# Optimization experiments

Hardware: AMD Instinct MI355X
Metric: run time of the kernel (lower is better)

## Reference

```python
import jax, jax.numpy as jnp
import numpy as np

EMB_DIM = 1024
N_HEADS = 16
HEAD_DIM = EMB_DIM // N_HEADS


def setup_inputs() -> dict:
    key = jax.random.key(0)
    ks = jax.random.split(key, 6)
    B, S, D = 2, 2048, EMB_DIM
    s = 1.0 / np.sqrt(D)
    return {
        "x": jax.random.normal(ks[0], (B, S, D), dtype=jnp.float32),
        "wq": jax.random.normal(ks[1], (D, D), dtype=jnp.float32) * s,
        "wk": jax.random.normal(ks[2], (D, D), dtype=jnp.float32) * s,
        "wv": jax.random.normal(ks[3], (D, D), dtype=jnp.float32) * s,
        "wo": jax.random.normal(ks[4], (D, D), dtype=jnp.float32) * s,
        "bo": jax.random.normal(ks[5], (D,), dtype=jnp.float32) * 0.01,
    }


def reference(x, wq, wk, wv, wo, bo):
    B, S, D = x.shape
    H, Hd = N_HEADS, HEAD_DIM
    # projections (torch Linear: y = x @ W.T; here weights are stored as [in, out])
    q = (x @ wq).reshape(B, S, H, Hd).transpose(0, 2, 1, 3)  # [B,H,S,Hd]
    k = (x @ wk).reshape(B, S, H, Hd).transpose(0, 2, 1, 3)
    v = (x @ wv).reshape(B, S, H, Hd).transpose(0, 2, 1, 3)
    scores = jnp.einsum("bhqd,bhkd->bhqk", q, k)  # [B,H,S,S]
    causal = jnp.tril(jnp.ones((S, S), dtype=bool))  # keep lower triangle
    scores = jnp.where(causal, scores, -jnp.inf)
    weights = jax.nn.softmax(scores / np.sqrt(Hd), axis=-1)
    ctx = jnp.einsum("bhqk,bhkd->bhqd", weights, v)  # [B,H,S,Hd]
    ctx = ctx.transpose(0, 2, 1, 3).reshape(B, S, D)
    return ctx @ wo + bo
```

## Files before the change

### kernel.cpp

```cpp
#include <hip/hip_runtime.h>
#include <hip/hip_bf16.h>

constexpr int B = 2, S = 2048, D = 1024, H = 16, Hd = 64;
constexpr int M = B * S;
constexpr int K = 1024;

typedef __attribute__((ext_vector_type(8))) short short8;
typedef __attribute__((ext_vector_type(4))) float f32x4;

__device__ __forceinline__ float bf2f(unsigned short u) {
    return __uint_as_float(((unsigned)u) << 16);
}
__device__ __forceinline__ unsigned short f2bf(float f) {
    unsigned u = __float_as_uint(f);
    u += 0x7FFF + ((u >> 16) & 1);
    return (unsigned short)(u >> 16);
}
__device__ __forceinline__ void gload_lds16(const unsigned short* g, unsigned short* l) {
    __builtin_amdgcn_global_load_lds(
        (const __attribute__((address_space(1))) void*)g,
        (__attribute__((address_space(3))) void*)l, 16, 0, 0);
}

__global__ __launch_bounds__(256) void convert_x_kernel(
    const float* __restrict__ x, unsigned short* __restrict__ xb)
{
    const size_t i = ((size_t)blockIdx.x * 256 + threadIdx.x) * 8;
    float4 a = *(const float4*)(x + i), b = *(const float4*)(x + i + 4);
    ushort4 u0 = {f2bf(a.x), f2bf(a.y), f2bf(a.z), f2bf(a.w)};
    ushort4 u1 = {f2bf(b.x), f2bf(b.y), f2bf(b.z), f2bf(b.w)};
    *(ushort4*)(xb + i) = u0;
    *(ushort4*)(xb + i + 4) = u1;
}

__global__ __launch_bounds__(256) void transpose_w_kernel(
    const float* __restrict__ wq, const float* __restrict__ wk,
    const float* __restrict__ wv, const float* __restrict__ wo,
    unsigned short* __restrict__ wqkv_t, unsigned short* __restrict__ wo_t)
{
    __shared__ float tile[64][65];
    const int z = blockIdx.z;
    const float* w = (z == 0) ? wq : (z == 1) ? wk : (z == 2) ? wv : wo;
    unsigned short* dst = (z == 3) ? wo_t : wqkv_t + (size_t)z * K * K;
    const int k0 = blockIdx.x * 64, n0 = blockIdx.y * 64;
    const int t = threadIdx.x;
    #pragma unroll
    for (int it = 0; it < 16; ++it) {
        int idx = t + it * 256;
        tile[idx >> 6][idx & 63] = w[(size_t)(k0 + (idx >> 6)) * K + n0 + (idx & 63)];
    }
    __syncthreads();
    #pragma unroll
    for (int it = 0; it < 16; ++it) {
        int idx = t + it * 256;
        int r = idx >> 6, c = idx & 63;
        dst[(size_t)(n0 + r) * K + k0 + c] = f2bf(tile[c][r]);
    }
}

__global__ __launch_bounds__(256) void qkv_mfma_kernel(
    const unsigned short* __restrict__ xa, const unsigned short* __restrict__ bt,
    unsigned short* __restrict__ q, unsigned short* __restrict__ k,
    unsigned short* __restrict__ vt)
{
    __shared__ unsigned short A_lds[2][128][32];
    __shared__ unsigned short B_lds[2][128][32];
    const int t = threadIdx.x, w = t >> 6, l = t & 63;
    const int lr = l & 15, lg = l >> 4;
    const int wm = w >> 1, wn = w & 1;
    const int m0 = blockIdx.x * 128, n0 = blockIdx.y * 128;
    const int srow = l >> 2, skofs = (l & 3) * 8;

    f32x4 acc[4][4];
    #pragma unroll
    for (int i = 0; i < 4; ++i)
        #pragma unroll
        for (int j = 0; j < 4; ++j) acc[i][j] = (f32x4){0.f, 0.f, 0.f, 0.f};

    #pragma unroll
    for (int p = 0; p < 2; ++p) {
        const int c = w * 2 + p;
        gload_lds16(xa + (size_t)(m0 + c * 16 + srow) * K + skofs, &A_lds[0][c * 16][0]);
        gload_lds16(bt + (size_t)(n0 + c * 16 + srow) * K + skofs, &B_lds[0][c * 16][0]);
    }
    __syncthreads();

    int cur = 0;
    for (int k0 = 0; k0 < K; k0 += 32) {
        if (k0 + 32 < K) {
            #pragma unroll
            for (int p = 0; p < 2; ++p) {
                const int c = w * 2 + p;
                gload_lds16(xa + (size_t)(m0 + c * 16 + srow) * K + k0 + 32 + skofs,
                            &A_lds[cur ^ 1][c * 16][0]);
                gload_lds16(bt + (size_t)(n0 + c * 16 + srow) * K + k0 + 32 + skofs,
                            &B_lds[cur ^ 1][c * 16][0]);
            }
        }
        short8 af[4], bf[4];
        #pragma unroll
        for (int i = 0; i < 4; ++i) af[i] = *(const short8*)&A_lds[cur][wm * 64 + i * 16 + lr][lg * 8];
        #pragma unroll
        for (int j = 0; j < 4; ++j) bf[j] = *(const short8*)&B_lds[cur][wn * 64 + j * 16 + lr][lg * 8];
        #pragma unroll
        for (int i = 0; i < 4; ++i)
            #pragma unroll
            for (int j = 0; j < 4; ++j)
                acc[i][j] = __builtin_amdgcn_mfma_f32_16x16x32_bf16(af[i], bf[j], acc[i][j], 0, 0, 0);
        __syncthreads();
        cur ^= 1;
    }

    const int z = (n0 >> 10);
    const float scale = (z == 0) ? 0.125f * 1.44269504f : 1.0f;
    #pragma unroll
    for (int i = 0; i < 4; ++i) {
        const int mbase = m0 + wm * 64 + i * 16 + lg * 4;
        #pragma unroll
        for (int j = 0; j < 4; ++j) {
            const int n = n0 + wn * 64 + j * 16 + lr;
            const int nn = n & 1023, hh = nn >> 6, hd = nn & 63;
            #pragma unroll
            for (int r = 0; r < 4; ++r) {
                const int mm = mbase + r, bb = mm >> 11, ss = mm & (S - 1);
                const unsigned short val = f2bf(acc[i][j][r] * scale);
                if (z == 0)      q[((size_t)(bb * H + hh) * S + ss) * Hd + hd] = val;
                else if (z == 1) k[((size_t)(bb * H + hh) * S + ss) * Hd + hd] = val;
                else             vt[((size_t)(bb * H + hh) * Hd + hd) * S + ss] = val;
            }
        }
    }
}

__global__ __launch_bounds__(256) void out_mfma_kernel(
    const unsigned short* __restrict__ a, const unsigned short* __restrict__ bt,
    const float* __restrict__ bias, float* __restrict__ out)
{
    __shared__ unsigned short A_lds[2][128][32];
    __shared__ unsigned short B_lds[2][128][32];
    const int t = threadIdx.x, w = t >> 6, l = t & 63;
    const int lr = l & 15, lg = l >> 4;
    const int wm = w >> 1, wn = w & 1;
    const int m0 = blockIdx.x * 128, n0 = blockIdx.y * 128;
    const int srow = l >> 2, skofs = (l & 3) * 8;

    f32x4 acc[4][4];
    #pragma unroll
    for (int i = 0; i < 4; ++i)
        #pragma unroll
        for (int j = 0; j < 4; ++j) acc[i][j] = (f32x4){0.f, 0.f, 0.f, 0.f};

    #pragma unroll
    for (int p = 0; p < 2; ++p) {
        const int c = w * 2 + p;
        gload_lds16(a  + (size_t)(m0 + c * 16 + srow) * K + skofs, &A_lds[0][c * 16][0]);
        gload_lds16(bt + (size_t)(n0 + c * 16 + srow) * K + skofs, &B_lds[0][c * 16][0]);
    }
    __syncthreads();

    int cur = 0;
    for (int k0 = 0; k0 < K; k0 += 32) {
        if (k0 + 32 < K) {
            #pragma unroll
            for (int p = 0; p < 2; ++p) {
                const int c = w * 2 + p;
                gload_lds16(a  + (size_t)(m0 + c * 16 + srow) * K + k0 + 32 + skofs,
                            &A_lds[cur ^ 1][c * 16][0]);
                gload_lds16(bt + (size_t)(n0 + c * 16 + srow) * K + k0 + 32 + skofs,
                            &B_lds[cur ^ 1][c * 16][0]);
            }
        }
        short8 af[4], bf[4];
        #pragma unroll
        for (int i = 0; i < 4; ++i) af[i] = *(const short8*)&A_lds[cur][wm * 64 + i * 16 + lr][lg * 8];
        #pragma unroll
        for (int j = 0; j < 4; ++j) bf[j] = *(const short8*)&B_lds[cur][wn * 64 + j * 16 + lr][lg * 8];
        #pragma unroll
        for (int i = 0; i < 4; ++i)
            #pragma unroll
            for (int j = 0; j < 4; ++j)
                acc[i][j] = __builtin_amdgcn_mfma_f32_16x16x32_bf16(af[i], bf[j], acc[i][j], 0, 0, 0);
        __syncthreads();
        cur ^= 1;
    }

    #pragma unroll
    for (int i = 0; i < 4; ++i) {
        const int mbase = m0 + wm * 64 + i * 16 + lg * 4;
        #pragma unroll
        for (int j = 0; j < 4; ++j) {
            const int n = n0 + wn * 64 + j * 16 + lr;
            const float bv = bias[n];
            #pragma unroll
            for (int r = 0; r < 4; ++r)
                out[(size_t)(mbase + r) * D + n] = acc[i][j][r] + bv;
        }
    }
}

__global__ __launch_bounds__(256) void attn_mfma_kernel(
    const unsigned short* __restrict__ q, const unsigned short* __restrict__ k,
    const unsigned short* __restrict__ vt, unsigned short* __restrict__ ctx)
{
    __shared__ unsigned short Kb[64 * 64];
    __shared__ unsigned short Vb[64 * 64];
    __shared__ unsigned short P_lds[4][16][72];
    const int t = threadIdx.x, w = t >> 6, l = t & 63;
    const int lr = l & 15, lg = l >> 4;

    const int bid = blockIdx.x;
    const int xcd = bid & 7;
    const int j   = bid >> 3;
    const int m   = j >> 5;
    const int c   = j & 31;
    const int bh  = xcd * 4 + m;
    const int bb  = bh >> 4, hh = bh & 15;
    const int qt  = (m & 1) ? (31 - c) : c;

    const int q0 = qt * 64 + w * 16;
    const int diag = qt;
    const size_t base  = (size_t)(bb * H + hh) * S * Hd;
    const size_t vbase = (size_t)(bb * H + hh) * Hd * S;

    const int srow0 = w * 16 + (l >> 3);
    const int scol  = (l & 7) * 8;

    short8 qf[2];
    #pragma unroll
    for (int cc = 0; cc < 2; ++cc)
        qf[cc] = *(const short8*)(q + base + (size_t)(q0 + lr) * Hd + cc * 32 + lg * 8);

    f32x4 accO[4];
    #pragma unroll
    for (int hb = 0; hb < 4; ++hb) accO[hb] = (f32x4){0.f, 0.f, 0.f, 0.f};
    float m_run = -INFINITY, l_run = 0.f;

    {
        short8 k0r[2], v0r[2];
        #pragma unroll
        for (int it = 0; it < 2; ++it) {
            const int row = srow0 + it * 8;
            k0r[it] = *(const short8*)(k + base + (size_t)row * Hd + scol);
            v0r[it] = *(const short8*)(vt + vbase + (size_t)row * S + scol);
        }
        #pragma unroll
        for (int it = 0; it < 2; ++it) {
            const int row = srow0 + it * 8;
            const int wc = (scol ^ ((row & 7) * 8));
            *(short8*)&Kb[row * 64 + wc] = k0r[it];
            *(short8*)&Vb[row * 64 + wc] = v0r[it];
        }
    }
    __syncthreads();

    for (int kt = 0; kt <= diag; ++kt) {
        short8 nK[2], nV[2];
        if (kt < diag) {
            const unsigned short* kg = k + base + (size_t)(kt + 1) * 64 * Hd;
            const unsigned short* vg = vt + vbase + (size_t)(kt + 1) * 64;
            #pragma unroll
            for (int it = 0; it < 2; ++it) {
                const int row = srow0 + it * 8;
                nK[it] = *(const short8*)(kg + (size_t)row * Hd + scol);
                nV[it] = *(const short8*)(vg + (size_t)row * S + scol);
            }
        }

        f32x4 accS[4];
        __builtin_amdgcn_s_setprio(1);
        #pragma unroll
        for (int kc = 0; kc < 4; ++kc) {
            accS[kc] = (f32x4){0.f, 0.f, 0.f, 0.f};
            const int krow = kc * 16 + lr;
            #pragma unroll
            for (int cc = 0; cc < 2; ++cc) {
                short8 kf = *(const short8*)&Kb[krow * 64 +
                    ((cc * 32 + lg * 8) ^ ((krow & 7) * 8))];
                accS[kc] = __builtin_amdgcn_mfma_f32_16x16x32_bf16(kf, qf[cc], accS[kc], 0, 0, 0);
            }
        }
        __builtin_amdgcn_s_setprio(0);

        float ps[16];
        #pragma unroll
        for (int kc = 0; kc < 4; ++kc)
            #pragma unroll
            for (int r = 0; r < 4; ++r) {
                float s = accS[kc][r];
                if (kt == diag && (kc * 16 + lg * 4 + r > w * 16 + lr)) s = -INFINITY;
                ps[kc * 4 + r] = s;
            }
        float m8[8];
        #pragma unroll
        for (int i = 0; i < 8; ++i) m8[i] = fmaxf(ps[i], ps[i + 8]);
        float m4a = fmaxf(m8[0], m8[4]), m4b = fmaxf(m8[1], m8[5]);
        float m4c = fmaxf(m8[2], m8[6]), m4d = fmaxf(m8[3], m8[7]);
        float mloc = fmaxf(fmaxf(m4a, m4b), fmaxf(m4c, m4d));
        mloc = fmaxf(mloc, __shfl_xor(mloc, 16));
        mloc = fmaxf(mloc, __shfl_xor(mloc, 32));

        const bool resc = __any(mloc > m_run + 8.f);
        const float mn = resc ? fmaxf(m_run, mloc) : m_run;

        #pragma unroll
        for (int i = 0; i < 16; ++i) ps[i] = exp2f(ps[i] - mn);
        float s8[8];
        #pragma unroll
        for (int i = 0; i < 8; ++i) s8[i] = ps[i] + ps[i + 8];
        float rs = ((s8[0] + s8[4]) + (s8[1] + s8[5])) +
                   ((s8[2] + s8[6]) + (s8[3] + s8[7]));
        rs += __shfl_xor(rs, 16);
        rs += __shfl_xor(rs, 32);

        if (resc) {
            const float sfc = exp2f(m_run - mn);
            l_run = l_run * sfc + rs;
            m_run = mn;
            #pragma unroll
            for (int hb = 0; hb < 4; ++hb)
                #pragma unroll
                for (int r = 0; r < 4; ++r) accO[hb][r] *= sfc;
        } else {
            l_run += rs;
        }

        #pragma unroll
        for (int kc = 0; kc < 4; ++kc) {
            uint2 pk;
            *(__hip_bfloat162*)&pk.x =
                __float22bfloat162_rn(make_float2(ps[kc * 4 + 0], ps[kc * 4 + 1]));
            *(__hip_bfloat162*)&pk.y =
                __float22bfloat162_rn(make_float2(ps[kc * 4 + 2], ps[kc * 4 + 3]));
            *(uint2*)&P_lds[w][lr][kc * 16 + lg * 4] = pk;
        }
        short8 pa[2];
        #pragma unroll
        for (int cc = 0; cc < 2; ++cc)
            pa[cc] = *(const short8*)&P_lds[w][lr][cc * 32 + lg * 8];

        __builtin_amdgcn_s_setprio(1);
        #pragma unroll
        for (int hb = 0; hb < 4; ++hb) {
            const int vrow = hb * 16 + lr;
            #pragma unroll
            for (int cc = 0; cc < 2; ++cc) {
                short8 vf = *(const short8*)&Vb[vrow * 64 +
                    ((cc * 32 + lg * 8) ^ ((vrow & 7) * 8))];
                accO[hb] = __builtin_amdgcn_mfma_f32_16x16x32_bf16(vf, pa[cc], accO[hb], 0, 0, 0);
            }
        }
        __builtin_amdgcn_s_setprio(0);

        __syncthreads();
        if (kt < diag) {
            #pragma unroll
            for (int it = 0; it < 2; ++it) {
                const int row = srow0 + it * 8;
                const int wc = (scol ^ ((row & 7) * 8));
                *(short8*)&Kb[row * 64 + wc] = nK[it];
                *(short8*)&Vb[row * 64 + wc] = nV[it];
            }
            __syncthreads();
        }
    }

    const float inv = 1.f / l_run;
    unsigned short* crow = ctx + (size_t)(bb * S + q0 + lr) * D + hh * Hd + lg * 4;
    #pragma unroll
    for (int hb = 0; hb < 4; ++hb) {
        ushort4 o;
        o.x = f2bf(accO[hb][0] * inv);
        o.y = f2bf(accO[hb][1] * inv);
        o.z = f2bf(accO[hb][2] * inv);
        o.w = f2bf(accO[hb][3] * inv);
        *(ushort4*)(crow + hb * 16) = o;
    }
}

extern "C" void kernel_launch(void* const* d_in, const int* in_sizes, int n_in,
                              void* d_out, int out_size, void* d_ws, size_t ws_size,
                              hipStream_t stream) {
    const float* x  = (const float*)d_in[0];
    const float* wq = (const float*)d_in[1];
    const float* wk = (const float*)d_in[2];
    const float* wv = (const float*)d_in[3];
    const float* wo = (const float*)d_in[4];
    const float* bo = (const float*)d_in[5];
    float* out = (float*)d_out;

    char* ws = (char*)d_ws;
    unsigned short* x_bf   = (unsigned short*)ws;
    unsigned short* q      = (unsigned short*)(ws + ((size_t)8  << 20));
    unsigned short* kk     = (unsigned short*)(ws + ((size_t)16 << 20));
    unsigned short* vt     = (unsigned short*)(ws + ((size_t)24 << 20));
    unsigned short* ctx    = x_bf;
    unsigned short* wqkv_t = (unsigned short*)(ws + ((size_t)32 << 20));
    unsigned short* wo_t   = (unsigned short*)(ws + ((size_t)38 << 20));

    convert_x_kernel<<<(M * K) / (256 * 8), 256, 0, stream>>>(x, x_bf);
    dim3 gtr(K / 64, K / 64, 4);
    transpose_w_kernel<<<gtr, 256, 0, stream>>>(wq, wk, wv, wo, wqkv_t, wo_t);

    dim3 gqkv(M / 128, 3072 / 128);
    qkv_mfma_kernel<<<gqkv, 256, 0, stream>>>(x_bf, wqkv_t, q, kk, vt);

    attn_mfma_kernel<<<1024, 256, 0, stream>>>(q, kk, vt, ctx);

    dim3 gout(M / 128, D / 128);
    out_mfma_kernel<<<gout, 256, 0, stream>>>(ctx, wo_t, bo, out);
}
```

Before: 130.9 us.

## Merge prep kernels, remap GEMM blocks per XCD, and double-buffer attention K/V

Folds the x conversion into the weight transpose kernel as an extra grid slice, which removes one launch. Both GEMMs switch to a 1D grid remapped so consecutive tiles land on the same XCD for L2 reuse. The attention kernel double-buffers K/V in LDS using direct global-to-LDS loads with a pre-swizzled source address, which removes the register staging and the second barrier per tile. It also swizzles the P scratch to avoid bank conflicts. Costs are more LDS per block, which may lower occupancy.

New measurement: 143.9 us. +9.9%, slower.

```diff
diff --git a/kernel.cpp b/kernel.cpp
--- a/kernel.cpp
+++ b/kernel.cpp
@@ -22,28 +22,33 @@
         (__attribute__((address_space(3))) void*)l, 16, 0, 0);
 }
 
-__global__ __launch_bounds__(256) void convert_x_kernel(
-    const float* __restrict__ x, unsigned short* __restrict__ xb)
-{
-    const size_t i = ((size_t)blockIdx.x * 256 + threadIdx.x) * 8;
-    float4 a = *(const float4*)(x + i), b = *(const float4*)(x + i + 4);
-    ushort4 u0 = {f2bf(a.x), f2bf(a.y), f2bf(a.z), f2bf(a.w)};
-    ushort4 u1 = {f2bf(b.x), f2bf(b.y), f2bf(b.z), f2bf(b.w)};
-    *(ushort4*)(xb + i) = u0;
-    *(ushort4*)(xb + i + 4) = u1;
-}
-
-__global__ __launch_bounds__(256) void transpose_w_kernel(
+__global__ __launch_bounds__(256) void prep_kernel(
+    const float* __restrict__ x,
     const float* __restrict__ wq, const float* __restrict__ wk,
     const float* __restrict__ wv, const float* __restrict__ wo,
+    unsigned short* __restrict__ xb,
     unsigned short* __restrict__ wqkv_t, unsigned short* __restrict__ wo_t)
 {
     __shared__ float tile[64][65];
     const int z = blockIdx.z;
+    const int t = threadIdx.x;
+    if (z == 4) {
+        const int bid = blockIdx.y * 16 + blockIdx.x;
+        const size_t base_i = ((size_t)bid * 256 + t) * 8;
+        #pragma unroll
+        for (int it = 0; it < 8; ++it) {
+            const size_t i = base_i + (size_t)it * 524288;
+            float4 a = *(const float4*)(x + i), b = *(const float4*)(x + i + 4);
+            ushort4 u0 = {f2bf(a.x), f2bf(a.y), f2bf(a.z), f2bf(a.w)};
+            ushort4 u1 = {f2bf(b.x), f2bf(b.y), f2bf(b.z), f2bf(b.w)};
+            *(ushort4*)(xb + i) = u0;
+            *(ushort4*)(xb + i + 4) = u1;
+        }
+        return;
+    }
     const float* w = (z == 0) ? wq : (z == 1) ? wk : (z == 2) ? wv : wo;
     unsigned short* dst = (z == 3) ? wo_t : wqkv_t + (size_t)z * K * K;
     const int k0 = blockIdx.x * 64, n0 = blockIdx.y * 64;
-    const int t = threadIdx.x;
     #pragma unroll
     for (int it = 0; it < 16; ++it) {
         int idx = t + it * 256;
@@ -68,7 +73,8 @@
     const int t = threadIdx.x, w = t >> 6, l = t & 63;
     const int lr = l & 15, lg = l >> 4;
     const int wm = w >> 1, wn = w & 1;
-    const int m0 = blockIdx.x * 128, n0 = blockIdx.y * 128;
+    const int lin = ((int)blockIdx.x & 7) * 96 + ((int)blockIdx.x >> 3);
+    const int m0 = (lin & 31) * 128, n0 = (lin >> 5) * 128;
     const int srow = l >> 2, skofs = (l & 3) * 8;
 
     f32x4 acc[4][4];
@@ -141,7 +147,8 @@
     const int t = threadIdx.x, w = t >> 6, l = t & 63;
     const int lr = l & 15, lg = l >> 4;
     const int wm = w >> 1, wn = w & 1;
-    const int m0 = blockIdx.x * 128, n0 = blockIdx.y * 128;
+    const int lin = ((int)blockIdx.x & 7) * 32 + ((int)blockIdx.x >> 3);
+    const int m0 = (lin & 31) * 128, n0 = (lin >> 5) * 128;
     const int srow = l >> 2, skofs = (l & 3) * 8;
 
     f32x4 acc[4][4];
@@ -198,13 +205,25 @@
     }
 }
 
+__device__ __forceinline__ void stage64(const unsigned short* __restrict__ g0,
+                                        size_t gstride, unsigned short* lbuf,
+                                        int w, int l) {
+    #pragma unroll
+    for (int it = 0; it < 2; ++it) {
+        const int chunk = w * 2 + it;
+        const int row = chunk * 8 + (l >> 3);
+        const int scol = ((l & 7) ^ (row & 7)) * 8;
+        gload_lds16(g0 + (size_t)row * gstride + scol, lbuf + chunk * 512);
+    }
+}
+
 __global__ __launch_bounds__(256) void attn_mfma_kernel(
     const unsigned short* __restrict__ q, const unsigned short* __restrict__ k,
     const unsigned short* __restrict__ vt, unsigned short* __restrict__ ctx)
 {
-    __shared__ unsigned short Kb[64 * 64];
-    __shared__ unsigned short Vb[64 * 64];
-    __shared__ unsigned short P_lds[4][16][72];
+    __shared__ unsigned short Kb[2][64 * 64];
+    __shared__ unsigned short Vb[2][64 * 64];
+    __shared__ unsigned short P_lds[4][16 * 64];
     const int t = threadIdx.x, w = t >> 6, l = t & 63;
     const int lr = l & 15, lg = l >> 4;
 
@@ -221,9 +240,7 @@
     const int diag = qt;
     const size_t base  = (size_t)(bb * H + hh) * S * Hd;
     const size_t vbase = (size_t)(bb * H + hh) * Hd * S;
-
-    const int srow0 = w * 16 + (l >> 3);
-    const int scol  = (l & 7) * 8;
+    const int pswz = (lr & 7) << 3;
 
     short8 qf[2];
     #pragma unroll
@@ -235,36 +252,19 @@
     for (int hb = 0; hb < 4; ++hb) accO[hb] = (f32x4){0.f, 0.f, 0.f, 0.f};
     float m_run = -INFINITY, l_run = 0.f;
 
-    {
-        short8 k0r[2], v0r[2];
-        #pragma unroll
-        for (int it = 0; it < 2; ++it) {
-            const int row = srow0 + it * 8;
-            k0r[it] = *(const short8*)(k + base + (size_t)row * Hd + scol);
-            v0r[it] = *(const short8*)(vt + vbase + (size_t)row * S + scol);
-        }
-        #pragma unroll
-        for (int it = 0; it < 2; ++it) {
-            const int row = srow0 + it * 8;
-            const int wc = (scol ^ ((row & 7) * 8));
-            *(short8*)&Kb[row * 64 + wc] = k0r[it];
-            *(short8*)&Vb[row * 64 + wc] = v0r[it];
-        }
-    }
+    stage64(k + base, Hd, Kb[0], w, l);
+    stage64(vt + vbase, S, Vb[0], w, l);
     __syncthreads();
 
+    int cur = 0;
     for (int kt = 0; kt <= diag; ++kt) {
-        short8 nK[2], nV[2];
         if (kt < diag) {
-            const unsigned short* kg = k + base + (size_t)(kt + 1) * 64 * Hd;
-            const unsigned short* vg = vt + vbase + (size_t)(kt + 1) * 64;
-            #pragma unroll
-            for (int it = 0; it < 2; ++it) {
-                const int row = srow0 + it * 8;
-                nK[it] = *(const short8*)(kg + (size_t)row * Hd + scol);
-                nV[it] = *(const short8*)(vg + (size_t)row * S + scol);
-            }
-        }
+            stage64(k + base + (size_t)(kt + 1) * 64 * Hd, Hd, Kb[cur ^ 1], w, l);
+            stage64(vt + vbase + (size_t)(kt + 1) * 64, S, Vb[cur ^ 1], w, l);
+        }
+
+        const unsigned short* Kc = Kb[cur];
+        const unsigned short* Vc = Vb[cur];
 
         f32x4 accS[4];
         __builtin_amdgcn_s_setprio(1);
@@ -274,7 +274,7 @@
             const int krow = kc * 16 + lr;
             #pragma unroll
             for (int cc = 0; cc < 2; ++cc) {
-                short8 kf = *(const short8*)&Kb[krow * 64 +
+                short8 kf = *(const short8*)&Kc[krow * 64 +
                     ((cc * 32 + lg * 8) ^ ((krow & 7) * 8))];
                 accS[kc] = __builtin_amdgcn_mfma_f32_16x16x32_bf16(kf, qf[cc], accS[kc], 0, 0, 0);
             }
@@ -331,12 +331,12 @@
                 __float22bfloat162_rn(make_float2(ps[kc * 4 + 0], ps[kc * 4 + 1]));
             *(__hip_bfloat162*)&pk.y =
                 __float22bfloat162_rn(make_float2(ps[kc * 4 + 2], ps[kc * 4 + 3]));
-            *(uint2*)&P_lds[w][lr][kc * 16 + lg * 4] = pk;
+            *(uint2*)&P_lds[w][lr * 64 + ((kc * 16 + lg * 4) ^ pswz)] = pk;
         }
         short8 pa[2];
         #pragma unroll
         for (int cc = 0; cc < 2; ++cc)
-            pa[cc] = *(const short8*)&P_lds[w][lr][cc * 32 + lg * 8];
+            pa[cc] = *(const short8*)&P_lds[w][lr * 64 + ((cc * 32 + lg * 8) ^ pswz)];
 
         __builtin_amdgcn_s_setprio(1);
         #pragma unroll
@@ -344,7 +344,7 @@
             const int vrow = hb * 16 + lr;
             #pragma unroll
             for (int cc = 0; cc < 2; ++cc) {
-                short8 vf = *(const short8*)&Vb[vrow * 64 +
+                short8 vf = *(const short8*)&Vc[vrow * 64 +
                     ((cc * 32 + lg * 8) ^ ((vrow & 7) * 8))];
                 accO[hb] = __builtin_amdgcn_mfma_f32_16x16x32_bf16(vf, pa[cc], accO[hb], 0, 0, 0);
             }
@@ -352,16 +352,7 @@
         __builtin_amdgcn_s_setprio(0);
 
         __syncthreads();
-        if (kt < diag) {
-            #pragma unroll
-            for (int it = 0; it < 2; ++it) {
-                const int row = srow0 + it * 8;
-                const int wc = (scol ^ ((row & 7) * 8));
-                *(short8*)&Kb[row * 64 + wc] = nK[it];
-                *(short8*)&Vb[row * 64 + wc] = nV[it];
-            }
-            __syncthreads();
-        }
+        cur ^= 1;
     }
 
     const float inv = 1.f / l_run;
@@ -397,15 +388,12 @@
     unsigned short* wqkv_t = (unsigned short*)(ws + ((size_t)32 << 20));
     unsigned short* wo_t   = (unsigned short*)(ws + ((size_t)38 << 20));
 
-    convert_x_kernel<<<(M * K) / (256 * 8), 256, 0, stream>>>(x, x_bf);
-    dim3 gtr(K / 64, K / 64, 4);
-    transpose_w_kernel<<<gtr, 256, 0, stream>>>(wq, wk, wv, wo, wqkv_t, wo_t);
-
-    dim3 gqkv(M / 128, 3072 / 128);
-    qkv_mfma_kernel<<<gqkv, 256, 0, stream>>>(x_bf, wqkv_t, q, kk, vt);
+    dim3 gprep(16, 16, 5);
+    prep_kernel<<<gprep, 256, 0, stream>>>(x, wq, wk, wv, wo, x_bf, wqkv_t, wo_t);
+
+    qkv_mfma_kernel<<<768, 256, 0, stream>>>(x_bf, wqkv_t, q, kk, vt);
 
     attn_mfma_kernel<<<1024, 256, 0, stream>>>(q, kk, vt, ctx);
 
-    dim3 gout(M / 128, D / 128);
-    out_mfma_kernel<<<gout, 256, 0, stream>>>(ctx, wo_t, bo, out);
-}
+    out_mfma_kernel<<<256, 256, 0, stream>>>(ctx, wo_t, bo, out);
+}
```
